# Kernel optimization log

Hardware: AMD Instinct MI355X
Metric: run time of the kernel (lower is better)

Reference implementation:

```python
import jax, jax.numpy as jnp
import numpy as np

H = 16  # head_count
NEG = -1e18


def setup_inputs() -> dict:
    key = jax.random.key(0)
    ks = jax.random.split(key, 10)
    B, S, D = 1, 2048, 1024
    inputs = jax.random.normal(ks[0], (B, S, D), dtype=jnp.float32)
    mask = jax.random.randint(ks[1], (B, S, S), 0, 2) == 1  # True => masked out
    std = 0.02
    Wq = jax.random.normal(ks[2], (D, D), jnp.float32) * std
    Wk = jax.random.normal(ks[3], (D, D), jnp.float32) * std
    Wv = jax.random.normal(ks[4], (D, D), jnp.float32) * std
    Wo = jax.random.normal(ks[5], (D, D), jnp.float32) * std
    bq = jnp.zeros((D,), jnp.float32)
    bk = jnp.zeros((D,), jnp.float32)
    bv = jnp.zeros((D,), jnp.float32)
    bo = jnp.zeros((D,), jnp.float32)
    return {"inputs": inputs, "mask": mask, "Wq": Wq, "bq": bq, "Wk": Wk,
            "bk": bk, "Wv": Wv, "bv": bv, "Wo": Wo, "bo": bo}


def reference(inputs, mask, Wq, bq, Wk, bk, Wv, bv, Wo, bo):
    B, S, D = inputs.shape
    dh = D // H
    scale = 1.0 / jnp.sqrt(jnp.asarray(dh, inputs.dtype))

    def shape(x):  # (B,S,D) -> (B,H,S,dh)
        return x.reshape(B, S, H, dh).transpose(0, 2, 1, 3)

    q = shape(inputs @ Wq.T + bq) * scale
    k = shape(inputs @ Wk.T + bk)
    v = shape(inputs @ Wv.T + bv)

    scores = jnp.einsum('bhqd,bhkd->bhqk', q, k).astype(jnp.float32)
    scores = jnp.where(mask[:, None, :, :], NEG, scores)
    attn = jax.nn.softmax(scores, axis=-1)
    # dropout p=0.0 -> identity
    ctx = jnp.einsum('bhqk,bhkd->bhqd', attn, v)
    ctx = ctx.transpose(0, 2, 1, 3).reshape(B, S, D)
    out = ctx @ Wo.T + bo
    return out, attn
```

## Files before the change

### kernel.cpp

```cpp
#include <hip/hip_runtime.h>
#include <hip/hip_bf16.h>

constexpr int S  = 2048;
constexpr int D  = 1024;
constexpr int H  = 16;
constexpr int DH = 64;

typedef __attribute__((ext_vector_type(8))) short short8;
typedef __attribute__((ext_vector_type(4))) short short4v;
typedef __attribute__((ext_vector_type(4))) float floatx4;

__device__ inline short f2b(float x) {
    union { float f; unsigned u; } v; v.f = x;
    unsigned r = v.u + 0x7FFFu + ((v.u >> 16) & 1u);
    return (short)(r >> 16);
}

__device__ inline void gl2lds16(const void* g, void* l) {
    __builtin_amdgcn_global_load_lds(
        (const __attribute__((address_space(1))) unsigned int*)g,
        (__attribute__((address_space(3))) unsigned int*)l, 16, 0, 0);
}

__global__ __launch_bounds__(256) void cvt_all_kernel(
    const float* __restrict__ X,  const float* __restrict__ Wq,
    const float* __restrict__ Wk, const float* __restrict__ Wv,
    const float* __restrict__ Wo,
    short* __restrict__ Xb,  short* __restrict__ Wqb,
    short* __restrict__ Wkb, short* __restrict__ Wvb,
    short* __restrict__ Wob)
{
    constexpr int SD = S * D, DD = D * D;
    int base = (blockIdx.x * 256 + threadIdx.x) * 4;
    const float* src; short* dst; int off;
    if (base < SD)               { src = X;  dst = Xb;  off = base; }
    else if (base < SD + DD)     { src = Wq; dst = Wqb; off = base - SD; }
    else if (base < SD + 2 * DD) { src = Wk; dst = Wkb; off = base - SD - DD; }
    else if (base < SD + 3 * DD) { src = Wv; dst = Wvb; off = base - SD - 2 * DD; }
    else                         { src = Wo; dst = Wob; off = base - SD - 3 * DD; }
    float4 v = *(const float4*)(src + off);
    short4v o;
    o.x = f2b(v.x); o.y = f2b(v.y); o.z = f2b(v.z); o.w = f2b(v.w);
    *(short4v*)(dst + off) = o;
}

__global__ __launch_bounds__(256) void maskpack_kernel(const int* __restrict__ mask,
                                                       unsigned long long* __restrict__ bits) {
    int gt   = blockIdx.x * 256 + threadIdx.x;
    int word = gt >> 6;
    int lane = gt & 63;
    int row  = word >> 5;
    int wcol = word & 31;
    int v = mask[(size_t)row * S + wcol * 64 + lane];
    unsigned long long b = __ballot(v != 0);
    if (lane == 0) bits[word] = b;
}

__device__ __forceinline__ void gemm_core(
    short* Asb, short* Bsb,
    const short* __restrict__ A, const short* __restrict__ B,
    const float* __restrict__ bias,
    short* __restrict__ o16, float* __restrict__ o32, int mode)
{
    int m0 = blockIdx.y * 128, n0 = blockIdx.x * 128;
    int tid = threadIdx.x;
    int w = tid >> 6, lane = tid & 63, quad = lane >> 4, l16 = lane & 15;
    int wm = w & 1, wn = w >> 1;

    const short* ag[2]; const short* bg[2]; int lo[2];
#pragma unroll
    for (int i = 0; i < 2; i++) {
        int c = tid + i * 256;
        int r = c >> 2, g4 = c & 3, sg = g4 ^ (r & 3);
        ag[i] = A + (size_t)(m0 + r) * D + sg * 8;
        bg[i] = B + (size_t)(n0 + r) * D + sg * 8;
        lo[i] = c * 8;
    }
#pragma unroll
    for (int i = 0; i < 2; i++) {
        gl2lds16(ag[i], &Asb[lo[i]]);
        gl2lds16(bg[i], &Bsb[lo[i]]);
    }

    floatx4 acc[4][4] = {};
    int gsw = quad ^ (l16 & 3);
    int cur = 0;

    for (int k0 = 0; k0 < D; k0 += 32) {
        __syncthreads();
        if (k0 + 32 < D) {
#pragma unroll
            for (int i = 0; i < 2; i++) {
                gl2lds16(ag[i] + k0 + 32, &Asb[(cur ^ 1) * 4096 + lo[i]]);
                gl2lds16(bg[i] + k0 + 32, &Bsb[(cur ^ 1) * 4096 + lo[i]]);
            }
        }
        short8 af[4], bf[4];
#pragma unroll
        for (int mt = 0; mt < 4; mt++)
            af[mt] = *(short8*)&Asb[cur * 4096 + (wm * 64 + mt * 16 + l16) * 32 + gsw * 8];
#pragma unroll
        for (int nt = 0; nt < 4; nt++)
            bf[nt] = *(short8*)&Bsb[cur * 4096 + (wn * 64 + nt * 16 + l16) * 32 + gsw * 8];
#pragma unroll
        for (int mt = 0; mt < 4; mt++)
#pragma unroll
            for (int nt = 0; nt < 4; nt++)
                acc[mt][nt] = __builtin_amdgcn_mfma_f32_16x16x32_bf16(af[mt], bf[nt], acc[mt][nt], 0, 0, 0);
        cur ^= 1;
    }

#pragma unroll
    for (int mt = 0; mt < 4; mt++)
#pragma unroll
        for (int nt = 0; nt < 4; nt++) {
            int col = n0 + wn * 64 + nt * 16 + l16;
            float bb = bias[col];
#pragma unroll
            for (int reg = 0; reg < 4; reg++) {
                int row = m0 + wm * 64 + mt * 16 + quad * 4 + reg;
                float v = acc[mt][nt][reg] + bb;
                if (mode == 0)      o16[(size_t)row * D + col] = f2b(v);
                else if (mode == 1) o16[(size_t)row * D + col] = f2b(v * 0.125f);
                else if (mode == 2) o16[(size_t)col * S + row] = f2b(v);
                else                o32[(size_t)row * D + col] = v;
            }
        }
}

__global__ __launch_bounds__(256) void gemm_qkv_kernel(
    const short* __restrict__ Xb,
    const short* __restrict__ Wqb, const short* __restrict__ Wkb,
    const short* __restrict__ Wvb,
    const float* __restrict__ bq, const float* __restrict__ bk,
    const float* __restrict__ bv,
    short* __restrict__ Qb, short* __restrict__ Kb, short* __restrict__ Vt)
{
    __shared__ short As[2 * 128 * 32];
    __shared__ short Bs[2 * 128 * 32];
    int z = blockIdx.z;
    const short* Bm   = (z == 0) ? Wqb : (z == 1) ? Wkb : Wvb;
    const float* bias = (z == 0) ? bq  : (z == 1) ? bk  : bv;
    short* out        = (z == 0) ? Qb  : (z == 1) ? Kb  : Vt;
    int mode          = (z == 0) ? 1   : (z == 1) ? 0   : 2;
    gemm_core(As, Bs, Xb, Bm, bias, out, nullptr, mode);
}

__global__ __launch_bounds__(256) void gemm_out_kernel(
    const short* __restrict__ A, const short* __restrict__ B,
    const float* __restrict__ bias, float* __restrict__ o32)
{
    __shared__ short As[2 * 128 * 32];
    __shared__ short Bs[2 * 128 * 32];
    gemm_core(As, Bs, A, B, bias, nullptr, o32, 3);
}

__global__ __launch_bounds__(256) void attn_kernel(
    const short* __restrict__ Qb,
    const short* __restrict__ Kb,
    const short* __restrict__ Vt,
    const unsigned long long* __restrict__ bits,
    float* __restrict__ attn,
    short* __restrict__ ctxb)
{
    __shared__ short Ks[2][64 * 64];
    __shared__ short Vs[2][64 * 64];
    __shared__ short Ps[64 * 72];
    int h = blockIdx.y, q0 = blockIdx.x * 64;
    int tid = threadIdx.x;
    int w = tid >> 6, lane = tid & 63, quad = lane >> 4, l16 = lane & 15;

    const short* kg[2]; const short* vg[2]; int lo[2];
#pragma unroll
    for (int i = 0; i < 2; i++) {
        int c = tid + i * 256;
        int r = c >> 3, c8 = c & 7, sg = c8 ^ (r & 7);
        kg[i] = Kb + (size_t)r * D + h * DH + sg * 8;
        vg[i] = Vt + (size_t)(h * DH + r) * S + sg * 8;
        lo[i] = c * 8;
    }

#pragma unroll
    for (int i = 0; i < 2; i++) gl2lds16(kg[i], &Ks[0][lo[i]]);
#pragma unroll
    for (int i = 0; i < 2; i++) {
        int c = tid + i * 256;
        int r = c >> 3, cc = (c & 7) * 8;
        *(short8*)&Ps[r * 72 + cc] = *(const short8*)(Qb + (size_t)(q0 + r) * D + h * DH + cc);
    }
    __syncthreads();
    short8 aq0 = *(short8*)&Ps[(w * 16 + l16) * 72 + quad * 8];
    short8 aq1 = *(short8*)&Ps[(w * 16 + l16) * 72 + 32 + quad * 8];

    int g0 = quad ^ (l16 & 7);
    int g1 = (quad + 4) ^ (l16 & 7);

    float m_r[4], l_r[4];
#pragma unroll
    for (int r = 0; r < 4; r++) { m_r[r] = -3.0e38f; l_r[r] = 0.0f; }

    int cur = 0;
    for (int kt = 0; kt < 32; kt++) {
        __syncthreads();
        if (kt + 1 < 32) {
#pragma unroll
            for (int i = 0; i < 2; i++)
                gl2lds16(kg[i] + (size_t)(kt + 1) * 64 * D, &Ks[cur ^ 1][lo[i]]);
        }
        floatx4 sc[4] = {};
#pragma unroll
        for (int nt = 0; nt < 4; nt++) {
            int row = nt * 16 + l16;
            short8 b0 = *(short8*)&Ks[cur][row * 64 + g0 * 8];
            short8 b1 = *(short8*)&Ks[cur][row * 64 + g1 * 8];
            sc[nt] = __builtin_amdgcn_mfma_f32_16x16x32_bf16(aq0, b0, sc[nt], 0, 0, 0);
            sc[nt] = __builtin_amdgcn_mfma_f32_16x16x32_bf16(aq1, b1, sc[nt], 0, 0, 0);
        }
#pragma unroll
        for (int reg = 0; reg < 4; reg++) {
            int q = q0 + w * 16 + quad * 4 + reg;
            unsigned long long w0 = bits[(size_t)q * 32 + kt];
            float sv[4], tmax = -3.0e38f;
#pragma unroll
            for (int nt = 0; nt < 4; nt++) {
                sv[nt] = ((w0 >> (nt * 16 + l16)) & 1ull) ? -1e18f : sc[nt][reg];
                tmax = fmaxf(tmax, sv[nt]);
            }
#pragma unroll
            for (int d = 1; d < 16; d <<= 1) tmax = fmaxf(tmax, __shfl_xor(tmax, d));
            float mn = fmaxf(m_r[reg], tmax);
            float ssum = 0.0f;
#pragma unroll
            for (int nt = 0; nt < 4; nt++) ssum += __expf(sv[nt] - mn);
#pragma unroll
            for (int d = 1; d < 16; d <<= 1) ssum += __shfl_xor(ssum, d);
            l_r[reg] = l_r[reg] * __expf(m_r[reg] - mn) + ssum;
            m_r[reg] = mn;
        }
        cur ^= 1;
    }
    float inv_l[4];
#pragma unroll
    for (int r = 0; r < 4; r++) inv_l[r] = 1.0f / l_r[r];

    floatx4 cacc[4] = {};
    float* attnh = attn + (size_t)h * S * S;

#pragma unroll
    for (int i = 0; i < 2; i++) {
        gl2lds16(kg[i], &Ks[0][lo[i]]);
        gl2lds16(vg[i], &Vs[0][lo[i]]);
    }
    cur = 0;

    for (int kt = 0; kt < 32; kt++) {
        __syncthreads();
        if (kt + 1 < 32) {
#pragma unroll
            for (int i = 0; i < 2; i++) {
                gl2lds16(kg[i] + (size_t)(kt + 1) * 64 * D, &Ks[cur ^ 1][lo[i]]);
                gl2lds16(vg[i] + (size_t)(kt + 1) * 64,     &Vs[cur ^ 1][lo[i]]);
            }
        }
        floatx4 sc[4] = {};
#pragma unroll
        for (int nt = 0; nt < 4; nt++) {
            int row = nt * 16 + l16;
            short8 b0 = *(short8*)&Ks[cur][row * 64 + g0 * 8];
            short8 b1 = *(short8*)&Ks[cur][row * 64 + g1 * 8];
            sc[nt] = __builtin_amdgcn_mfma_f32_16x16x32_bf16(aq0, b0, sc[nt], 0, 0, 0);
            sc[nt] = __builtin_amdgcn_mfma_f32_16x16x32_bf16(aq1, b1, sc[nt], 0, 0, 0);
        }
        int k0g = kt * 64;
#pragma unroll
        for (int reg = 0; reg < 4; reg++) {
            int q = q0 + w * 16 + quad * 4 + reg;
            unsigned long long w0 = bits[(size_t)q * 32 + kt];
            float* arow = attnh + (size_t)q * S + k0g;
#pragma unroll
            for (int nt = 0; nt < 4; nt++) {
                float svv = ((w0 >> (nt * 16 + l16)) & 1ull) ? -1e18f : sc[nt][reg];
                float p = __expf(svv - m_r[reg]) * inv_l[reg];
                arow[nt * 16 + l16] = p;
                Ps[(w * 16 + quad * 4 + reg) * 72 + nt * 16 + l16] = f2b(p);
            }
        }
        short8 pa[2];
#pragma unroll
        for (int kc = 0; kc < 2; kc++)
            pa[kc] = *(short8*)&Ps[(w * 16 + l16) * 72 + kc * 32 + quad * 8];
#pragma unroll
        for (int nt = 0; nt < 4; nt++) {
            int d = nt * 16 + l16;
#pragma unroll
            for (int kc = 0; kc < 2; kc++) {
                int g = (kc * 4 + quad) ^ (l16 & 7);
                short8 vb = *(short8*)&Vs[cur][d * 64 + g * 8];
                cacc[nt] = __builtin_amdgcn_mfma_f32_16x16x32_bf16(pa[kc], vb, cacc[nt], 0, 0, 0);
            }
        }
        cur ^= 1;
    }

#pragma unroll
    for (int nt = 0; nt < 4; nt++)
#pragma unroll
        for (int reg = 0; reg < 4; reg++) {
            int q = q0 + w * 16 + quad * 4 + reg;
            ctxb[(size_t)q * D + h * DH + nt * 16 + l16] = f2b(cacc[nt][reg]);
        }
}

extern "C" void kernel_launch(void* const* d_in, const int* in_sizes, int n_in,
                              void* d_out, int out_size, void* d_ws, size_t ws_size,
                              hipStream_t stream)
{
    const float* X    = (const float*)d_in[0];
    const int*   mask = (const int*)d_in[1];
    const float* Wq   = (const float*)d_in[2];
    const float* bq   = (const float*)d_in[3];
    const float* Wk   = (const float*)d_in[4];
    const float* bk   = (const float*)d_in[5];
    const float* Wv   = (const float*)d_in[6];
    const float* bv   = (const float*)d_in[7];
    const float* Wo   = (const float*)d_in[8];
    const float* bo   = (const float*)d_in[9];

    float* out  = (float*)d_out;
    float* attn = out + (size_t)S * D;

    char* ws = (char*)d_ws;
    short* Xb   = (short*)ws;  ws += (size_t)S * D * 2;
    short* Wqb  = (short*)ws;  ws += (size_t)D * D * 2;
    short* Wkb  = (short*)ws;  ws += (size_t)D * D * 2;
    short* Wvb  = (short*)ws;  ws += (size_t)D * D * 2;
    short* Wob  = (short*)ws;  ws += (size_t)D * D * 2;
    short* Qb   = (short*)ws;  ws += (size_t)S * D * 2;
    short* Kb   = (short*)ws;  ws += (size_t)S * D * 2;
    short* Vt   = (short*)ws;  ws += (size_t)S * D * 2;
    short* ctxb = (short*)ws;  ws += (size_t)S * D * 2;
    unsigned long long* bits = (unsigned long long*)ws;

    dim3 blk(256);

    cvt_all_kernel<<<dim3((S * D + 4 * D * D) / 1024), blk, 0, stream>>>(
        X, Wq, Wk, Wv, Wo, Xb, Wqb, Wkb, Wvb, Wob);
    maskpack_kernel<<<dim3((S * S) / 256), blk, 0, stream>>>(mask, bits);

    gemm_qkv_kernel<<<dim3(D / 128, S / 128, 3), blk, 0, stream>>>(
        Xb, Wqb, Wkb, Wvb, bq, bk, bv, Qb, Kb, Vt);

    attn_kernel<<<dim3(S / 64, H), blk, 0, stream>>>(Qb, Kb, Vt, bits, attn, ctxb);

    gemm_out_kernel<<<dim3(D / 128, S / 128), blk, 0, stream>>>(ctxb, Wob, bo, out);
}
```

Before: 479.0 us.

## Triple-buffer GEMM and attention loads, use exp2 softmax, shrink GEMM tile

The GEMM and attention loops move from double-buffered loads with full __syncthreads to a three-slot ring prefetched two tiles ahead, synchronised with explicit vmcnt waits and raw barriers. The GEMM tile is reduced from 128x128 to 128x64, which doubles the block count. The Q scale now folds in log2(e) so the softmax can use hardware exp2. The first pass keeps per-lane running max and sum and reduces them across lanes only once at the end, replacing a shuffle reduction on every tile. MFMA sections are wrapped in setprio, and each mask word is loaded once per tile before the MFMAs. The hand-written waitcnt logic is fragile and could let a tile be read before its load completes.

```diff
diff --git a/kernel.cpp b/kernel.cpp
--- a/kernel.cpp
+++ b/kernel.cpp
@@ -10,11 +10,23 @@
 typedef __attribute__((ext_vector_type(4))) short short4v;
 typedef __attribute__((ext_vector_type(4))) float floatx4;
 
+#define QSCALE 0.18033688011112042f
+
 __device__ inline short f2b(float x) {
     union { float f; unsigned u; } v; v.f = x;
     unsigned r = v.u + 0x7FFFu + ((v.u >> 16) & 1u);
     return (short)(r >> 16);
 }
+
+__device__ __forceinline__ float e2(float x) { return __builtin_amdgcn_exp2f(x); }
+
+template<int N> __device__ __forceinline__ void wait_vm() {
+    asm volatile("s_waitcnt vmcnt(%0)" :: "n"(N) : "memory");
+}
+__device__ __forceinline__ void wait_lgkm0() {
+    asm volatile("s_waitcnt lgkmcnt(0)" ::: "memory");
+}
+__device__ __forceinline__ void bar() { __builtin_amdgcn_s_barrier(); }
 
 __device__ inline void gl2lds16(const void* g, void* l) {
     __builtin_amdgcn_global_load_lds(
@@ -56,72 +68,84 @@
     if (lane == 0) bits[word] = b;
 }
 
+constexpr int BM = 128, BN = 64, BK = 32, RING = 3;
+constexpr int ASZ = BM * BK;
+constexpr int BSZ = BN * BK;
+constexpr int GL  = 3;
+
 __device__ __forceinline__ void gemm_core(
     short* Asb, short* Bsb,
     const short* __restrict__ A, const short* __restrict__ B,
     const float* __restrict__ bias,
     short* __restrict__ o16, float* __restrict__ o32, int mode)
 {
-    int m0 = blockIdx.y * 128, n0 = blockIdx.x * 128;
+    int m0 = blockIdx.y * BM, n0 = blockIdx.x * BN;
     int tid = threadIdx.x;
     int w = tid >> 6, lane = tid & 63, quad = lane >> 4, l16 = lane & 15;
     int wm = w & 1, wn = w >> 1;
 
-    const short* ag[2]; const short* bg[2]; int lo[2];
+    const short* ag[2]; int alo[2];
 #pragma unroll
     for (int i = 0; i < 2; i++) {
         int c = tid + i * 256;
         int r = c >> 2, g4 = c & 3, sg = g4 ^ (r & 3);
         ag[i] = A + (size_t)(m0 + r) * D + sg * 8;
-        bg[i] = B + (size_t)(n0 + r) * D + sg * 8;
-        lo[i] = c * 8;
-    }
-#pragma unroll
-    for (int i = 0; i < 2; i++) {
-        gl2lds16(ag[i], &Asb[lo[i]]);
-        gl2lds16(bg[i], &Bsb[lo[i]]);
-    }
-
-    floatx4 acc[4][4] = {};
+        alo[i] = c * 8;
+    }
+    const short* bg; int blo;
+    {
+        int c = tid;
+        int r = c >> 2, g4 = c & 3, sg = g4 ^ (r & 3);
+        bg = B + (size_t)(n0 + r) * D + sg * 8;
+        blo = c * 8;
+    }
+
+    auto stage = [&](int t) {
+        int sl = t % RING;
+#pragma unroll
+        for (int i = 0; i < 2; i++) gl2lds16(ag[i] + t * BK, &Asb[sl * ASZ + alo[i]]);
+        gl2lds16(bg + t * BK, &Bsb[sl * BSZ + blo]);
+    };
+
+    stage(0); stage(1);
+
+    floatx4 acc[4][2] = {};
     int gsw = quad ^ (l16 & 3);
-    int cur = 0;
-
-    for (int k0 = 0; k0 < D; k0 += 32) {
-        __syncthreads();
-        if (k0 + 32 < D) {
-#pragma unroll
-            for (int i = 0; i < 2; i++) {
-                gl2lds16(ag[i] + k0 + 32, &Asb[(cur ^ 1) * 4096 + lo[i]]);
-                gl2lds16(bg[i] + k0 + 32, &Bsb[(cur ^ 1) * 4096 + lo[i]]);
-            }
-        }
-        short8 af[4], bf[4];
+    constexpr int NT = D / BK;
+
+    for (int j = 0; j < NT; j++) {
+        if (j < NT - 1) wait_vm<GL>(); else wait_vm<0>();
+        bar();
+        if (j + 2 < NT) stage(j + 2);
+        int sl = j % RING;
+        short8 af[4], bf[2];
 #pragma unroll
         for (int mt = 0; mt < 4; mt++)
-            af[mt] = *(short8*)&Asb[cur * 4096 + (wm * 64 + mt * 16 + l16) * 32 + gsw * 8];
-#pragma unroll
-        for (int nt = 0; nt < 4; nt++)
-            bf[nt] = *(short8*)&Bsb[cur * 4096 + (wn * 64 + nt * 16 + l16) * 32 + gsw * 8];
+            af[mt] = *(short8*)&Asb[sl * ASZ + (wm * 64 + mt * 16 + l16) * BK + gsw * 8];
+#pragma unroll
+        for (int nt = 0; nt < 2; nt++)
+            bf[nt] = *(short8*)&Bsb[sl * BSZ + (wn * 32 + nt * 16 + l16) * BK + gsw * 8];
+        __builtin_amdgcn_s_setprio(1);
 #pragma unroll
         for (int mt = 0; mt < 4; mt++)
 #pragma unroll
-            for (int nt = 0; nt < 4; nt++)
+            for (int nt = 0; nt < 2; nt++)
                 acc[mt][nt] = __builtin_amdgcn_mfma_f32_16x16x32_bf16(af[mt], bf[nt], acc[mt][nt], 0, 0, 0);
-        cur ^= 1;
+        __builtin_amdgcn_s_setprio(0);
     }
 
 #pragma unroll
     for (int mt = 0; mt < 4; mt++)
 #pragma unroll
-        for (int nt = 0; nt < 4; nt++) {
-            int col = n0 + wn * 64 + nt * 16 + l16;
+        for (int nt = 0; nt < 2; nt++) {
+            int col = n0 + wn * 32 + nt * 16 + l16;
             float bb = bias[col];
 #pragma unroll
             for (int reg = 0; reg < 4; reg++) {
                 int row = m0 + wm * 64 + mt * 16 + quad * 4 + reg;
                 float v = acc[mt][nt][reg] + bb;
                 if (mode == 0)      o16[(size_t)row * D + col] = f2b(v);
-                else if (mode == 1) o16[(size_t)row * D + col] = f2b(v * 0.125f);
+                else if (mode == 1) o16[(size_t)row * D + col] = f2b(v * QSCALE);
                 else if (mode == 2) o16[(size_t)col * S + row] = f2b(v);
                 else                o32[(size_t)row * D + col] = v;
             }
@@ -136,8 +160,8 @@
     const float* __restrict__ bv,
     short* __restrict__ Qb, short* __restrict__ Kb, short* __restrict__ Vt)
 {
-    __shared__ short As[2 * 128 * 32];
-    __shared__ short Bs[2 * 128 * 32];
+    __shared__ short As[RING * ASZ];
+    __shared__ short Bs[RING * BSZ];
     int z = blockIdx.z;
     const short* Bm   = (z == 0) ? Wqb : (z == 1) ? Wkb : Wvb;
     const float* bias = (z == 0) ? bq  : (z == 1) ? bk  : bv;
@@ -150,8 +174,8 @@
     const short* __restrict__ A, const short* __restrict__ B,
     const float* __restrict__ bias, float* __restrict__ o32)
 {
-    __shared__ short As[2 * 128 * 32];
-    __shared__ short Bs[2 * 128 * 32];
+    __shared__ short As[RING * ASZ];
+    __shared__ short Bs[RING * BSZ];
     gemm_core(As, Bs, A, B, bias, nullptr, o32, 3);
 }
 
@@ -163,8 +187,8 @@
     float* __restrict__ attn,
     short* __restrict__ ctxb)
 {
-    __shared__ short Ks[2][64 * 64];
-    __shared__ short Vs[2][64 * 64];
+    __shared__ short Ks[RING][64 * 64];
+    __shared__ short Vs[RING][64 * 64];
     __shared__ short Ps[64 * 72];
     int h = blockIdx.y, q0 = blockIdx.x * 64;
     int tid = threadIdx.x;
@@ -183,104 +207,129 @@
 #pragma unroll
     for (int i = 0; i < 2; i++) gl2lds16(kg[i], &Ks[0][lo[i]]);
 #pragma unroll
+    for (int i = 0; i < 2; i++) gl2lds16(kg[i] + (size_t)64 * D, &Ks[1][lo[i]]);
+#pragma unroll
     for (int i = 0; i < 2; i++) {
         int c = tid + i * 256;
         int r = c >> 3, cc = (c & 7) * 8;
         *(short8*)&Ps[r * 72 + cc] = *(const short8*)(Qb + (size_t)(q0 + r) * D + h * DH + cc);
     }
-    __syncthreads();
+    wait_lgkm0();
+    bar();
     short8 aq0 = *(short8*)&Ps[(w * 16 + l16) * 72 + quad * 8];
     short8 aq1 = *(short8*)&Ps[(w * 16 + l16) * 72 + 32 + quad * 8];
 
     int g0 = quad ^ (l16 & 7);
     int g1 = (quad + 4) ^ (l16 & 7);
 
-    float m_r[4], l_r[4];
-#pragma unroll
-    for (int r = 0; r < 4; r++) { m_r[r] = -3.0e38f; l_r[r] = 0.0f; }
-
-    int cur = 0;
-    for (int kt = 0; kt < 32; kt++) {
-        __syncthreads();
-        if (kt + 1 < 32) {
+    float m_l[4], l_l[4];
+#pragma unroll
+    for (int r = 0; r < 4; r++) { m_l[r] = -3.0e38f; l_l[r] = 0.0f; }
+
+    for (int j = 0; j < 32; j++) {
+        if (j < 31) wait_vm<2>(); else wait_vm<0>();
+        bar();
+        unsigned long long bw[4];
+#pragma unroll
+        for (int reg = 0; reg < 4; reg++) {
+            int q = q0 + w * 16 + quad * 4 + reg;
+            bw[reg] = bits[(size_t)q * 32 + j];
+        }
+        if (j + 2 < 32) {
+            int sp = (j + 2) % RING;
 #pragma unroll
             for (int i = 0; i < 2; i++)
-                gl2lds16(kg[i] + (size_t)(kt + 1) * 64 * D, &Ks[cur ^ 1][lo[i]]);
-        }
+                gl2lds16(kg[i] + (size_t)(j + 2) * 64 * D, &Ks[sp][lo[i]]);
+        }
+        int sl = j % RING;
         floatx4 sc[4] = {};
+        __builtin_amdgcn_s_setprio(1);
 #pragma unroll
         for (int nt = 0; nt < 4; nt++) {
             int row = nt * 16 + l16;
-            short8 b0 = *(short8*)&Ks[cur][row * 64 + g0 * 8];
-            short8 b1 = *(short8*)&Ks[cur][row * 64 + g1 * 8];
+            short8 b0 = *(short8*)&Ks[sl][row * 64 + g0 * 8];
+            short8 b1 = *(short8*)&Ks[sl][row * 64 + g1 * 8];
             sc[nt] = __builtin_amdgcn_mfma_f32_16x16x32_bf16(aq0, b0, sc[nt], 0, 0, 0);
             sc[nt] = __builtin_amdgcn_mfma_f32_16x16x32_bf16(aq1, b1, sc[nt], 0, 0, 0);
         }
+        __builtin_amdgcn_s_setprio(0);
+#pragma unroll
+        for (int reg = 0; reg < 4; reg++) {
+            float sv[4];
+#pragma unroll
+            for (int nt = 0; nt < 4; nt++)
+                sv[nt] = ((bw[reg] >> (nt * 16 + l16)) & 1ull) ? -1e18f : sc[nt][reg];
+            float tmax = fmaxf(fmaxf(sv[0], sv[1]), fmaxf(sv[2], sv[3]));
+            float mn = fmaxf(m_l[reg], tmax);
+            float s = e2(sv[0] - mn) + e2(sv[1] - mn) + e2(sv[2] - mn) + e2(sv[3] - mn);
+            l_l[reg] = l_l[reg] * e2(m_l[reg] - mn) + s;
+            m_l[reg] = mn;
+        }
+    }
+    float m_r[4], inv_l[4];
+#pragma unroll
+    for (int reg = 0; reg < 4; reg++) {
+        float m = m_l[reg], l = l_l[reg];
+#pragma unroll
+        for (int d = 1; d < 16; d <<= 1) {
+            float om = __shfl_xor(m, d);
+            float ol = __shfl_xor(l, d);
+            float mn = fmaxf(m, om);
+            l = l * e2(m - mn) + ol * e2(om - mn);
+            m = mn;
+        }
+        m_r[reg] = m;
+        inv_l[reg] = 1.0f / l;
+    }
+
+    bar();
+
+#pragma unroll
+    for (int i = 0; i < 2; i++) { gl2lds16(kg[i], &Ks[0][lo[i]]); gl2lds16(vg[i], &Vs[0][lo[i]]); }
+#pragma unroll
+    for (int i = 0; i < 2; i++) { gl2lds16(kg[i] + (size_t)64 * D, &Ks[1][lo[i]]); gl2lds16(vg[i] + 64, &Vs[1][lo[i]]); }
+
+    floatx4 cacc[4] = {};
+    float* attnh = attn + (size_t)h * S * S;
+
+    for (int j = 0; j < 32; j++) {
+        if (j < 31) wait_vm<4>(); else wait_vm<0>();
+        bar();
+        unsigned long long bw[4];
 #pragma unroll
         for (int reg = 0; reg < 4; reg++) {
             int q = q0 + w * 16 + quad * 4 + reg;
-            unsigned long long w0 = bits[(size_t)q * 32 + kt];
-            float sv[4], tmax = -3.0e38f;
-#pragma unroll
-            for (int nt = 0; nt < 4; nt++) {
-                sv[nt] = ((w0 >> (nt * 16 + l16)) & 1ull) ? -1e18f : sc[nt][reg];
-                tmax = fmaxf(tmax, sv[nt]);
+            bw[reg] = bits[(size_t)q * 32 + j];
+        }
+        if (j + 2 < 32) {
+            int sp = (j + 2) % RING;
+#pragma unroll
+            for (int i = 0; i < 2; i++) {
+                gl2lds16(kg[i] + (size_t)(j + 2) * 64 * D, &Ks[sp][lo[i]]);
+                gl2lds16(vg[i] + (size_t)(j + 2) * 64,     &Vs[sp][lo[i]]);
             }
-#pragma unroll
-            for (int d = 1; d < 16; d <<= 1) tmax = fmaxf(tmax, __shfl_xor(tmax, d));
-            float mn = fmaxf(m_r[reg], tmax);
-            float ssum = 0.0f;
-#pragma unroll
-            for (int nt = 0; nt < 4; nt++) ssum += __expf(sv[nt] - mn);
-#pragma unroll
-            for (int d = 1; d < 16; d <<= 1) ssum += __shfl_xor(ssum, d);
-            l_r[reg] = l_r[reg] * __expf(m_r[reg] - mn) + ssum;
-            m_r[reg] = mn;
-        }
-        cur ^= 1;
-    }
-    float inv_l[4];
-#pragma unroll
-    for (int r = 0; r < 4; r++) inv_l[r] = 1.0f / l_r[r];
-
-    floatx4 cacc[4] = {};
-    float* attnh = attn + (size_t)h * S * S;
-
-#pragma unroll
-    for (int i = 0; i < 2; i++) {
-        gl2lds16(kg[i], &Ks[0][lo[i]]);
-        gl2lds16(vg[i], &Vs[0][lo[i]]);
-    }
-    cur = 0;
-
-    for (int kt = 0; kt < 32; kt++) {
-        __syncthreads();
-        if (kt + 1 < 32) {
-#pragma unroll
-            for (int i = 0; i < 2; i++) {
-                gl2lds16(kg[i] + (size_t)(kt + 1) * 64 * D, &Ks[cur ^ 1][lo[i]]);
-                gl2lds16(vg[i] + (size_t)(kt + 1) * 64,     &Vs[cur ^ 1][lo[i]]);
-            }
-        }
+        }
+        int sl = j % RING;
         floatx4 sc[4] = {};
+        __builtin_amdgcn_s_setprio(1);
 #pragma unroll
         for (int nt = 0; nt < 4; nt++) {
             int row = nt * 16 + l16;
-            short8 b0 = *(short8*)&Ks[cur][row * 64 + g0 * 8];
-            short8 b1 = *(short8*)&Ks[cur][row * 64 + g1 * 8];
+            short8 b0 = *(short8*)&Ks[sl][row * 64 + g0 * 8];
+            short8 b1 = *(short8*)&Ks[sl][row * 64 + g1 * 8];
             sc[nt] = __builtin_amdgcn_mfma_f32_16x16x32_bf16(aq0, b0, sc[nt], 0, 0, 0);
             sc[nt] = __builtin_amdgcn_mfma_f32_16x16x32_bf16(aq1, b1, sc[nt], 0, 0, 0);
         }
-        int k0g = kt * 64;
+        __builtin_amdgcn_s_setprio(0);
+        int k0g = j * 64;
 #pragma unroll
         for (int reg = 0; reg < 4; reg++) {
             int q = q0 + w * 16 + quad * 4 + reg;
-            unsigned long long w0 = bits[(size_t)q * 32 + kt];
             float* arow = attnh + (size_t)q * S + k0g;
 #pragma unroll
             for (int nt = 0; nt < 4; nt++) {
-                float svv = ((w0 >> (nt * 16 + l16)) & 1ull) ? -1e18f : sc[nt][reg];
-                float p = __expf(svv - m_r[reg]) * inv_l[reg];
+                float svv = ((bw[reg] >> (nt * 16 + l16)) & 1ull) ? -1e18f : sc[nt][reg];
+                float p = e2(svv - m_r[reg]) * inv_l[reg];
                 arow[nt * 16 + l16] = p;
                 Ps[(w * 16 + quad * 4 + reg) * 72 + nt * 16 + l16] = f2b(p);
             }
@@ -289,17 +338,18 @@
 #pragma unroll
         for (int kc = 0; kc < 2; kc++)
             pa[kc] = *(short8*)&Ps[(w * 16 + l16) * 72 + kc * 32 + quad * 8];
+        __builtin_amdgcn_s_setprio(1);
 #pragma unroll
         for (int nt = 0; nt < 4; nt++) {
             int d = nt * 16 + l16;
 #pragma unroll
             for (int kc = 0; kc < 2; kc++) {
                 int g = (kc * 4 + quad) ^ (l16 & 7);
-                short8 vb = *(short8*)&Vs[cur][d * 64 + g * 8];
+                short8 vb = *(short8*)&Vs[sl][d * 64 + g * 8];
                 cacc[nt] = __builtin_amdgcn_mfma_f32_16x16x32_bf16(pa[kc], vb, cacc[nt], 0, 0, 0);
             }
         }
-        cur ^= 1;
+        __builtin_amdgcn_s_setprio(0);
     }
 
 #pragma unroll
@@ -347,10 +397,10 @@
         X, Wq, Wk, Wv, Wo, Xb, Wqb, Wkb, Wvb, Wob);
     maskpack_kernel<<<dim3((S * S) / 256), blk, 0, stream>>>(mask, bits);
 
-    gemm_qkv_kernel<<<dim3(D / 128, S / 128, 3), blk, 0, stream>>>(
+    gemm_qkv_kernel<<<dim3(D / BN, S / BM, 3), blk, 0, stream>>>(
         Xb, Wqb, Wkb, Wvb, bq, bk, bv, Qb, Kb, Vt);
 
     attn_kernel<<<dim3(S / 64, H), blk, 0, stream>>>(Qb, Kb, Vt, bits, attn, ctxb);
 
-    gemm_out_kernel<<<dim3(D / 128, S / 128), blk, 0, stream>>>(ctxb, Wob, bo, out);
-}
+    gemm_out_kernel<<<dim3(D / BN, S / BM), blk, 0, stream>>>(ctxb, Wob, bo, out);
+}
```

Result: faster. 428.1 us (-10.6%).
